# Performance work log

Measured on AMD Instinct MI355X. Metric: run time of the kernel, lower is better.

The kernel has to match this reference:

```python
import jax, jax.numpy as jnp
import numpy as np

BETA = 0.5

def gelu(x):
    return jax.nn.gelu(x, approximate=False)  # torch F.gelu default is exact erf

def setup_inputs() -> dict:
    key = jax.random.key(0)
    ks = jax.random.split(key, 10)
    N, F, PH, P, D, H, C, E = 50000, 128, 64, 8, 4, 128, 10, 1600000
    s = 0.05
    return {
        "x": jax.random.normal(ks[0], (N, F), jnp.float32),
        "W_proj": jax.random.normal(ks[1], (PH, F), jnp.float32) * s,
        "b_proj": jnp.zeros((PH,), jnp.float32),
        "W_x": jax.random.normal(ks[2], (H, F), jnp.float32) * s,
        "b_x": jnp.zeros((H,), jnp.float32),
        "W_path": jax.random.normal(ks[3], (H, D * PH), jnp.float32) * s,
        "b_path": jnp.zeros((H,), jnp.float32),
        "W_A": jax.random.normal(ks[4], (H, N), jnp.float32) * s,
        "b_A": jnp.zeros((H,), jnp.float32),
        "W_end": jax.random.normal(ks[5], (C, H), jnp.float32) * s,
        "b_end": jnp.zeros((C,), jnp.float32),
        "index": jax.random.randint(ks[6], (N, P, D), 0, N, jnp.int64)
                 if jax.config.jax_enable_x64 else jax.random.randint(ks[6], (N, P, D), 0, N, jnp.int32),
        "edge_index": jax.random.randint(ks[7], (2, E), 0, N, jnp.int32),
    }

def reference(x, W_proj, b_proj, W_x, b_x, W_path, b_path, W_A, b_A, W_end, b_end, index, edge_index):
    N = x.shape[0]
    # path projection then per-node path gather: [N, P, D, PH]
    pp = x @ W_proj.T + b_proj
    path = pp[index]
    Np, P, D, PH = path.shape
    # node MLP (dropout off in eval)
    h = gelu(x @ W_x.T + b_x)  # [N, H]
    # concat path encoder: [N, P, D*PH] -> [N, P, H]
    pi = gelu(path.reshape(Np, P, D * PH) @ W_path.T + b_path)
    # dot-product path attention with softmax over path dim
    att = jax.nn.softmax(jnp.einsum('nh,nph->np', h, pi), axis=-1)
    path_agg = jnp.einsum('np,nph->nh', att, pi)
    # sparse adjacency (COO, weights=1) times Linear weight: A @ W_A.T + b_A
    M = W_A.T  # [N, H]
    A_x = jax.ops.segment_sum(M[edge_index[1]], edge_index[0], num_segments=N) + b_A
    out = (1.0 - BETA) * (path_agg + h) + BETA * A_x
    out = gelu(out)
    return out @ W_end.T + b_end
```

## Files before the change

kernel.cpp:

```cpp
#include <hip/hip_runtime.h>
#include <hip/hip_bf16.h>
#include <math.h>

#define NF   128
#define NPH  64
#define NP   8
#define ND   4
#define NH   128
#define NC   10
#define BCAP 2560

typedef __bf16 bf16;
typedef __attribute__((ext_vector_type(4))) __bf16 bf16x4;
typedef __attribute__((ext_vector_type(8))) __bf16 bf16x8;
typedef __attribute__((ext_vector_type(4))) float f32x4;

template<int CTRL>
__device__ __forceinline__ float dpp_add(float x) {
    int t = __builtin_amdgcn_update_dpp(0, __float_as_int(x), CTRL, 0xf, 0xf, false);
    return x + __int_as_float(t);
}
__device__ __forceinline__ float row16_sum(float x) {
    x = dpp_add<0x121>(x);
    x = dpp_add<0x122>(x);
    x = dpp_add<0x124>(x);
    x = dpp_add<0x128>(x);
    return x;
}

__device__ __forceinline__ float gelu_fast(float x) {
    float z = fabsf(x) * 0.70710678118654752f;
    float t = __builtin_amdgcn_rcpf(1.0f + 0.47047f * z);
    float poly = t * (0.3480242f + t * (-0.0958798f + t * 0.7478556f));
    float erfv = 1.0f - poly * __expf(-z * z);
    float s = copysignf(erfv, x);
    return 0.5f * x * (1.0f + s);
}

#define GLOAD_LDS16(g, l)                                                     \
    __builtin_amdgcn_global_load_lds(                                         \
        (const __attribute__((address_space(1))) unsigned int*)(g),           \
        (__attribute__((address_space(3))) unsigned int*)(l), 16, 0, 0)

__device__ __forceinline__ bf16x8 cvt8(float4 a, float4 b) {
    bf16x8 r;
    r[0] = (bf16)a.x; r[1] = (bf16)a.y; r[2] = (bf16)a.z; r[3] = (bf16)a.w;
    r[4] = (bf16)b.x; r[5] = (bf16)b.y; r[6] = (bf16)b.z; r[7] = (bf16)b.w;
    return r;
}

__global__ __launch_bounds__(256) void k_front(
    const float* __restrict__ x,
    const float* __restrict__ Wproj, const float* __restrict__ bproj,
    const float* __restrict__ Wx,    const float* __restrict__ bx,
    bf16* __restrict__ pp, float* __restrict__ h,
    const float* __restrict__ WA, bf16* __restrict__ Mb,
    const int* __restrict__ esrc, const int* __restrict__ edst,
    int* __restrict__ gcur, unsigned* __restrict__ pairs,
    int N, int E, int nbuck, int nbP, int nbT)
{
    __shared__ alignas(16) char smem[33280];
    const int tid = threadIdx.x;

    const int bid = blockIdx.x;
    const int two = 2 * nbP;
    int cls, idx;
    if (bid < two) { cls = bid & 1; idx = bid >> 1; }
    else           { cls = 1; idx = nbP + (bid - two); }

    if (cls == 0) {
        bf16* x_s = (bf16*)smem;
        const int w = tid >> 6, l = tid & 63;
        const int c = l & 15, g = l >> 4;

        bf16x8 bfr[3][4];
        float bias[3];
        #pragma unroll
        for (int t = 0; t < 3; ++t) {
            int ch = (w * 3 + t) * 16 + c;
            const float* wr = (ch < NPH) ? &Wproj[(size_t)ch * NF]
                                         : &Wx[(size_t)(ch - NPH) * NF];
            bias[t] = (ch < NPH) ? bproj[ch] : bx[ch - NPH];
            #pragma unroll
            for (int ks = 0; ks < 4; ++ks) {
                const float* src = wr + ks * 32 + g * 8;
                bfr[t][ks] = cvt8(*(const float4*)src, *(const float4*)(src + 4));
            }
        }

        const int n0 = idx * 64;
        #pragma unroll
        for (int rr = 0; rr < 8; ++rr) {
            int id  = rr * 256 + tid;
            int row = id >> 5, c4 = id & 31;
            float4 v = make_float4(0.f, 0.f, 0.f, 0.f);
            if (n0 + row < N) v = *(const float4*)&x[(size_t)(n0 + row) * NF + c4 * 4];
            bf16x4 o;
            o[0] = (bf16)v.x; o[1] = (bf16)v.y; o[2] = (bf16)v.z; o[3] = (bf16)v.w;
            *(bf16x4*)&x_s[row * 136 + c4 * 4] = o;
        }
        __syncthreads();

        f32x4 acc[4][3] = {};
        #pragma unroll
        for (int rt = 0; rt < 4; ++rt)
            #pragma unroll
            for (int ks = 0; ks < 4; ++ks) {
                bf16x8 a = *(const bf16x8*)&x_s[(rt * 16 + c) * 136 + ks * 32 + g * 8];
                #pragma unroll
                for (int t = 0; t < 3; ++t)
                    acc[rt][t] = __builtin_amdgcn_mfma_f32_16x16x32_bf16(
                        a, bfr[t][ks], acc[rt][t], 0, 0, 0);
            }

        #pragma unroll
        for (int rt = 0; rt < 4; ++rt) {
            #pragma unroll
            for (int t = 0; t < 3; ++t) {
                int ch = (w * 3 + t) * 16 + c;
                #pragma unroll
                for (int i = 0; i < 4; ++i) {
                    int n = n0 + rt * 16 + g * 4 + i;
                    if (n >= N) continue;
                    float v = acc[rt][t][i] + bias[t];
                    if (ch < NPH) pp[(size_t)n * NPH + ch] = (bf16)v;
                    else          h[(size_t)n * NH + (ch - NPH)] = gelu_fast(v);
                }
            }
        }
    } else if (idx < nbT) {
        float* tt = (float*)smem;
        const int n0 = idx * 64;
        const int w = tid >> 6, l = tid & 63;
        #pragma unroll
        for (int rep = 0; rep < 32; ++rep) {
            int hh = rep * 4 + w;
            int n  = n0 + l;
            tt[hh * 65 + l] = (n < N) ? WA[(size_t)hh * N + n] : 0.f;
        }
        __syncthreads();
        #pragma unroll
        for (int rep = 0; rep < 32; ++rep) {
            int n_l = rep * 2 + (tid >> 7);
            int n   = n0 + n_l;
            if (n < N) Mb[(size_t)n * NH + (tid & 127)] = (bf16)tt[(tid & 127) * 65 + n_l];
        }
    } else {
        int* cnt  = (int*)smem;
        int* bofs = cnt + 800;
        const int tile = (idx - nbT) * 4096;
        for (int i = tid; i < nbuck; i += 256) cnt[i] = 0;
        __syncthreads();
        #pragma unroll
        for (int k = 0; k < 16; ++k) {
            int i = tile + k * 256 + tid;
            if (i < E) atomicAdd(&cnt[esrc[i] >> 6], 1);
        }
        __syncthreads();
        for (int i = tid; i < nbuck; i += 256) {
            int c = cnt[i];
            bofs[i] = c ? atomicAdd(&gcur[i], c) : 0;
            cnt[i] = 0;
        }
        __syncthreads();
        #pragma unroll
        for (int k = 0; k < 16; ++k) {
            int i = tile + k * 256 + tid;
            if (i < E) {
                int s = esrc[i], b = s >> 6;
                int r = atomicAdd(&cnt[b], 1);
                pairs[(size_t)b * BCAP + bofs[b] + r] =
                    ((unsigned)(s & 63) << 16) | (unsigned)edst[i];
            }
        }
    }
}

__global__ __launch_bounds__(256) void k_ax(
    const unsigned* __restrict__ pairs, const int* __restrict__ gcur,
    const bf16* __restrict__ Mb, const float* __restrict__ bA,
    float* __restrict__ axbuf2, int N)
{
    __shared__ int hist[64], sc[64], cur[64];
    __shared__ unsigned short dstl[BCAP];
    const int bid = blockIdx.x;
    const int ct  = bid & 3;
    const int b   = bid >> 2;
    const int t   = threadIdx.x;
    const int cnt = gcur[b];
    const unsigned* pb = pairs + (size_t)b * BCAP;

    if (t < 64) hist[t] = 0;
    __syncthreads();
    for (int j = t; j < cnt; j += 256)
        atomicAdd(&hist[pb[j] >> 16], 1);
    __syncthreads();
    if (t < 64) sc[t] = hist[t];
    __syncthreads();
    for (int off = 1; off < 64; off <<= 1) {
        int u = (t < 64 && t >= off) ? sc[t - off] : 0;
        __syncthreads();
        if (t < 64) sc[t] += u;
        __syncthreads();
    }
    if (t < 64) cur[t] = sc[t] - hist[t];
    __syncthreads();
    for (int j = t; j < cnt; j += 256) {
        unsigned p = pb[j];
        int pos = atomicAdd(&cur[p >> 16], 1);
        dstl[pos] = (unsigned short)(p & 0xffffu);
    }
    __syncthreads();

    const int w = t >> 6, l = t & 63;
    const int e = l >> 4, q = l & 15;
    const unsigned* Mu32 = (const unsigned*)Mb;
    const int dwbase = ct * 16;
    const int chb = ct * 32;
    const int nb0 = b * 64;
    const float bA0 = bA[chb + q * 2];
    const float bA1 = bA[chb + q * 2 + 1];

    #pragma unroll 1
    for (int it = 0; it < 16; ++it) {
        const int node = it * 4 + w;
        const int hi2 = sc[node];
        int j = hi2 - hist[node];
        float a0 = 0.f, a1 = 0.f;
        for (; j + 16 <= hi2; j += 16) {
            int d0 = dstl[j + e], d1 = dstl[j + 4 + e];
            int d2 = dstl[j + 8 + e], d3 = dstl[j + 12 + e];
            unsigned v0 = Mu32[(size_t)d0 * 64 + dwbase + q];
            unsigned v1 = Mu32[(size_t)d1 * 64 + dwbase + q];
            unsigned v2 = Mu32[(size_t)d2 * 64 + dwbase + q];
            unsigned v3 = Mu32[(size_t)d3 * 64 + dwbase + q];
            a0 += __uint_as_float(v0 << 16) + __uint_as_float(v1 << 16) +
                  __uint_as_float(v2 << 16) + __uint_as_float(v3 << 16);
            a1 += __uint_as_float(v0 & 0xffff0000u) + __uint_as_float(v1 & 0xffff0000u) +
                  __uint_as_float(v2 & 0xffff0000u) + __uint_as_float(v3 & 0xffff0000u);
        }
        for (; j + 4 <= hi2; j += 4) {
            int d0 = dstl[j + e];
            unsigned v0 = Mu32[(size_t)d0 * 64 + dwbase + q];
            a0 += __uint_as_float(v0 << 16);
            a1 += __uint_as_float(v0 & 0xffff0000u);
        }
        if (j + e < hi2) {
            int d0 = dstl[j + e];
            unsigned v0 = Mu32[(size_t)d0 * 64 + dwbase + q];
            a0 += __uint_as_float(v0 << 16);
            a1 += __uint_as_float(v0 & 0xffff0000u);
        }
        a0 += __shfl_xor(a0, 16, 64);  a0 += __shfl_xor(a0, 32, 64);
        a1 += __shfl_xor(a1, 16, 64);  a1 += __shfl_xor(a1, 32, 64);
        const int n = nb0 + node;
        if (l < 16 && n < N) {
            float2 o;
            o.x = 0.5f * (a0 + bA0);
            o.y = 0.5f * (a1 + bA1);
            *(float2*)&axbuf2[(size_t)n * NH + chb + q * 2] = o;
        }
    }
}

__global__ __launch_bounds__(256, 3) void k_path(
    const bf16* __restrict__ pp, const float* __restrict__ h,
    const float* __restrict__ Wpath, const float* __restrict__ bpath,
    const int* __restrict__ index, float* __restrict__ aggbuf,
    int N, int nrounds)
{
    __shared__ alignas(16) char smem[37376];
    bf16*  path_s = (bf16*)smem;
    float* h_sf   = (float*)(smem + 32768);
    float* s_red  = (float*)(smem + 36864);

    const int tid = threadIdx.x;
    const int w   = tid >> 6;
    const int l   = tid & 63;
    const int c   = l & 15;
    const int g   = l >> 4;
    const int nl  = g >> 1;

    bf16x8 bfrag[2][8];
    #pragma unroll
    for (int ht = 0; ht < 2; ++ht) {
        int hg = (w * 2 + ht) * 16 + c;
        #pragma unroll
        for (int ks = 0; ks < 8; ++ks) {
            const float* src = &Wpath[(size_t)hg * 256 + ks * 32 + g * 8];
            bfrag[ht][ks] = cvt8(*(const float4*)src, *(const float4*)(src + 4));
        }
    }
    const float bp0 = bpath[(w * 2 + 0) * 16 + c];
    const float bp1 = bpath[(w * 2 + 1) * 16 + c];

    auto stage = [&](int round, int b) {
        const int n0 = round * 4;
        #pragma unroll
        for (int rr = 0; rr < 4; ++rr) {
            int id  = rr * 256 + tid;
            int row = id >> 5;
            int cc  = id & 31;
            int ls  = cc ^ (row & 7);
            int d   = ls >> 3, q = ls & 7;
            int nn  = row >> 3, p = row & 7;
            int idx = index[(size_t)(n0 + nn) * (NP * ND) + p * ND + d];
            GLOAD_LDS16(pp + (size_t)idx * NPH + q * 8, &path_s[b * 8192 + id * 8]);
        }
        if (tid < 128) {
            int node = tid >> 5, q = tid & 31;
            GLOAD_LDS16(&h[(size_t)(n0 + node) * NH + q * 4],
                        &h_sf[(b * 4 + node) * 128 + q * 4]);
        }
    };

    int r = blockIdx.x;
    const int G = gridDim.x;
    if (r < nrounds) stage(r, 0);
    int buf = 0;

    for (; r < nrounds; r += G) {
        const int n0 = r * 4;
        __syncthreads();
        if (r + G < nrounds) stage(r + G, buf ^ 1);

        f32x4 acc[2][2] = {};
        #pragma unroll
        for (int rt = 0; rt < 2; ++rt) {
            const int rowbase = buf * 8192 + (rt * 16 + c) * 256;
            #pragma unroll
            for (int ks = 0; ks < 8; ++ks) {
                int chunk = (ks * 4 + g) ^ (c & 7);
                bf16x8 a = *(const bf16x8*)&path_s[rowbase + chunk * 8];
                acc[rt][0] = __builtin_amdgcn_mfma_f32_16x16x32_bf16(
                    a, bfrag[0][ks], acc[rt][0], 0, 0, 0);
                acc[rt][1] = __builtin_amdgcn_mfma_f32_16x16x32_bf16(
                    a, bfrag[1][ks], acc[rt][1], 0, 0, 0);
            }
        }

        float pi[2][2][4];
        #pragma unroll
        for (int rt = 0; rt < 2; ++rt) {
            const float hv0 = h_sf[(buf * 4 + rt * 2 + nl) * 128 + w * 32 + c];
            const float hv1 = h_sf[(buf * 4 + rt * 2 + nl) * 128 + w * 32 + 16 + c];
            float sp[4];
            #pragma unroll
            for (int i = 0; i < 4; ++i) {
                pi[rt][0][i] = gelu_fast(acc[rt][0][i] + bp0);
                pi[rt][1][i] = gelu_fast(acc[rt][1][i] + bp1);
                sp[i] = hv0 * pi[rt][0][i] + hv1 * pi[rt][1][i];
            }
            #pragma unroll
            for (int i = 0; i < 4; ++i) sp[i] = row16_sum(sp[i]);
            float v = (c == 0) ? sp[0] : (c == 1) ? sp[1] : (c == 2) ? sp[2] : sp[3];
            if (c < 4) s_red[w * 32 + rt * 16 + g * 4 + c] = v;
        }

        __builtin_amdgcn_sched_barrier(0);
        asm volatile("s_waitcnt lgkmcnt(0)" ::: "memory");
        __builtin_amdgcn_s_barrier();
        __builtin_amdgcn_sched_barrier(0);

        #pragma unroll
        for (int rt = 0; rt < 2; ++rt) {
            float4 r0 = *(const float4*)&s_red[0 * 32 + rt * 16 + g * 4];
            float4 r1 = *(const float4*)&s_red[1 * 32 + rt * 16 + g * 4];
            float4 r2 = *(const float4*)&s_red[2 * 32 + rt * 16 + g * 4];
            float4 r3 = *(const float4*)&s_red[3 * 32 + rt * 16 + g * 4];
            float st[4];
            st[0] = r0.x + r1.x + r2.x + r3.x;
            st[1] = r0.y + r1.y + r2.y + r3.y;
            st[2] = r0.z + r1.z + r2.z + r3.z;
            st[3] = r0.w + r1.w + r2.w + r3.w;
            float m4 = fmaxf(fmaxf(st[0], st[1]), fmaxf(st[2], st[3]));
            float m  = fmaxf(m4, __shfl_xor(m4, 16, 64));
            float e[4], s4 = 0.f;
            #pragma unroll
            for (int i = 0; i < 4; ++i) { e[i] = __expf(st[i] - m); s4 += e[i]; }
            float den = s4 + __shfl_xor(s4, 16, 64);
            const float inv = __builtin_amdgcn_rcpf(den);

            float pa0 = 0.f, pa1 = 0.f;
            #pragma unroll
            for (int i = 0; i < 4; ++i) {
                pa0 += e[i] * pi[rt][0][i];
                pa1 += e[i] * pi[rt][1][i];
            }
            pa0 = (pa0 + __shfl_xor(pa0, 16, 64)) * inv;
            pa1 = (pa1 + __shfl_xor(pa1, 16, 64)) * inv;

            if (!(g & 1)) {
                int n = n0 + rt * 2 + nl;
                const float hv0 = h_sf[(buf * 4 + rt * 2 + nl) * 128 + w * 32 + c];
                const float hv1 = h_sf[(buf * 4 + rt * 2 + nl) * 128 + w * 32 + 16 + c];
                aggbuf[(size_t)n * NH + w * 32 + c]      = 0.5f * (pa0 + hv0);
                aggbuf[(size_t)n * NH + w * 32 + 16 + c] = 0.5f * (pa1 + hv1);
            }
        }
        buf ^= 1;
    }
}

__global__ __launch_bounds__(256) void k_fin(
    const float* __restrict__ aggbuf, const float* __restrict__ axbuf2,
    const float* __restrict__ Wend, const float* __restrict__ bend,
    float* __restrict__ out, int N)
{
    __shared__ float wend_s[NC][128];
    __shared__ float bend_s[NC];
    const int tid = threadIdx.x;
    for (int id = tid; id < NC * 128; id += 256) wend_s[id >> 7][id & 127] = Wend[id];
    if (tid < NC) bend_s[tid] = bend[tid];
    __syncthreads();

    const int w = tid >> 6, l = tid & 63;
    const int n = blockIdx.x * 4 + w;
    if (n >= N) return;
    const int q = l & 15;

    float4 agA = *(const float4*)&aggbuf[(size_t)n * NH + q * 8];
    float4 agB = *(const float4*)&aggbuf[(size_t)n * NH + q * 8 + 4];
    float4 axA = *(const float4*)&axbuf2[(size_t)n * NH + q * 8];
    float4 axB = *(const float4*)&axbuf2[(size_t)n * NH + q * 8 + 4];
    float gg[8];
    gg[0] = gelu_fast(agA.x + axA.x);
    gg[1] = gelu_fast(agA.y + axA.y);
    gg[2] = gelu_fast(agA.z + axA.z);
    gg[3] = gelu_fast(agA.w + axA.w);
    gg[4] = gelu_fast(agB.x + axB.x);
    gg[5] = gelu_fast(agB.y + axB.y);
    gg[6] = gelu_fast(agB.z + axB.z);
    gg[7] = gelu_fast(agB.w + axB.w);

    float part[NC];
    #pragma unroll
    for (int cc = 0; cc < NC; ++cc) {
        float p = 0.f;
        #pragma unroll
        for (int k = 0; k < 8; ++k) p += gg[k] * wend_s[cc][q * 8 + k];
        part[cc] = row16_sum(p);
    }

    float r = part[0];
    #pragma unroll
    for (int cc = 1; cc < NC; ++cc) r = (l == cc) ? part[cc] : r;
    if (l < NC) out[(size_t)n * NC + l] = r + bend_s[l];
}

extern "C" void kernel_launch(void* const* d_in, const int* in_sizes, int n_in,
                              void* d_out, int out_size, void* d_ws, size_t ws_size,
                              hipStream_t stream)
{
    const float* x     = (const float*)d_in[0];
    const float* Wproj = (const float*)d_in[1];
    const float* bproj = (const float*)d_in[2];
    const float* Wx    = (const float*)d_in[3];
    const float* bx    = (const float*)d_in[4];
    const float* Wpath = (const float*)d_in[5];
    const float* bpath = (const float*)d_in[6];
    const float* WA    = (const float*)d_in[7];
    const float* bA    = (const float*)d_in[8];
    const float* Wend  = (const float*)d_in[9];
    const float* bend  = (const float*)d_in[10];
    const int*   index = (const int*)d_in[11];
    const int*   eidx  = (const int*)d_in[12];

    const int N = in_sizes[0] / NF;
    const int E = in_sizes[12] / 2;
    const int* esrc = eidx;
    const int* edst = eidx + E;
    const int nbuck = (N + 63) >> 6;

    char* p = (char*)d_ws;
    auto alloc = [&](size_t bytes) {
        char* r = p;
        p += (bytes + 255) & ~(size_t)255;
        return r;
    };
    bf16*     pp     = (bf16*)alloc((size_t)N * NPH * sizeof(bf16));
    float*    h      = (float*)alloc((size_t)N * NH * sizeof(float));
    float*    aggbuf = (float*)alloc((size_t)N * NH * sizeof(float));
    float*    axbuf2 = (float*)alloc((size_t)N * NH * sizeof(float));
    bf16*     Mb     = (bf16*)alloc((size_t)N * NH * sizeof(bf16));
    unsigned* pairs  = (unsigned*)alloc((size_t)nbuck * BCAP * sizeof(unsigned));
    int*      gcur   = (int*)alloc((size_t)nbuck * sizeof(int));

    const int nbP = (N + 63) / 64;
    const int nbT = (N + 63) / 64;
    const int nbB = (E + 4095) / 4096;
    const int NPATH = 1024;
    const int nrounds = N / 4;

    hipMemsetAsync(gcur, 0, (size_t)nbuck * sizeof(int), stream);
    k_front<<<nbP + nbT + nbB, 256, 0, stream>>>(
        x, Wproj, bproj, Wx, bx, pp, h, WA, Mb, esrc, edst, gcur, pairs,
        N, E, nbuck, nbP, nbT);
    k_ax<<<nbuck * 4, 256, 0, stream>>>(pairs, gcur, Mb, bA, axbuf2, N);
    k_path<<<NPATH, 256, 0, stream>>>(pp, h, Wpath, bpath, index, aggbuf, N, nrounds);
    k_fin<<<(N + 3) / 4, 256, 0, stream>>>(aggbuf, axbuf2, Wend, bend,
                                           (float*)d_out, N);
}
```

Baseline: 250.2 us.

## Fuse final GELU and output projection into path kernel; split front kernel

```diff
diff --git a/kernel.cpp b/kernel.cpp
--- a/kernel.cpp
+++ b/kernel.cpp
@@ -49,129 +49,132 @@
     return r;
 }
 
-__global__ __launch_bounds__(256) void k_front(
+__global__ __launch_bounds__(256) void k_proj(
     const float* __restrict__ x,
     const float* __restrict__ Wproj, const float* __restrict__ bproj,
     const float* __restrict__ Wx,    const float* __restrict__ bx,
-    bf16* __restrict__ pp, float* __restrict__ h,
-    const float* __restrict__ WA, bf16* __restrict__ Mb,
+    bf16* __restrict__ pp, float* __restrict__ h, int N)
+{
+    __shared__ alignas(16) bf16 x_s[64 * 136];
+    const int tid = threadIdx.x;
+    const int w = tid >> 6, l = tid & 63;
+    const int c = l & 15, g = l >> 4;
+
+    bf16x8 bfr[3][4];
+    float bias[3];
+    #pragma unroll
+    for (int t = 0; t < 3; ++t) {
+        int ch = (w * 3 + t) * 16 + c;
+        const float* wr = (ch < NPH) ? &Wproj[(size_t)ch * NF]
+                                     : &Wx[(size_t)(ch - NPH) * NF];
+        bias[t] = (ch < NPH) ? bproj[ch] : bx[ch - NPH];
+        #pragma unroll
+        for (int ks = 0; ks < 4; ++ks) {
+            const float* src = wr + ks * 32 + g * 8;
+            bfr[t][ks] = cvt8(*(const float4*)src, *(const float4*)(src + 4));
+        }
+    }
+
+    const int n0 = blockIdx.x * 64;
+    #pragma unroll
+    for (int rr = 0; rr < 8; ++rr) {
+        int id  = rr * 256 + tid;
+        int row = id >> 5, c4 = id & 31;
+        float4 v = make_float4(0.f, 0.f, 0.f, 0.f);
+        if (n0 + row < N) v = *(const float4*)&x[(size_t)(n0 + row) * NF + c4 * 4];
+        bf16x4 o;
+        o[0] = (bf16)v.x; o[1] = (bf16)v.y; o[2] = (bf16)v.z; o[3] = (bf16)v.w;
+        *(bf16x4*)&x_s[row * 136 + c4 * 4] = o;
+    }
+    __syncthreads();
+
+    f32x4 acc[4][3] = {};
+    #pragma unroll
+    for (int rt = 0; rt < 4; ++rt)
+        #pragma unroll
+        for (int ks = 0; ks < 4; ++ks) {
+            bf16x8 a = *(const bf16x8*)&x_s[(rt * 16 + c) * 136 + ks * 32 + g * 8];
+            #pragma unroll
+            for (int t = 0; t < 3; ++t)
+                acc[rt][t] = __builtin_amdgcn_mfma_f32_16x16x32_bf16(
+                    a, bfr[t][ks], acc[rt][t], 0, 0, 0);
+        }
+
+    #pragma unroll
+    for (int rt = 0; rt < 4; ++rt) {
+        #pragma unroll
+        for (int t = 0; t < 3; ++t) {
+            int ch = (w * 3 + t) * 16 + c;
+            #pragma unroll
+            for (int i = 0; i < 4; ++i) {
+                int n = n0 + rt * 16 + g * 4 + i;
+                if (n >= N) continue;
+                float v = acc[rt][t][i] + bias[t];
+                if (ch < NPH) pp[(size_t)n * NPH + ch] = (bf16)v;
+                else          h[(size_t)n * NH + (ch - NPH)] = gelu_fast(v);
+            }
+        }
+    }
+}
+
+__global__ __launch_bounds__(256) void k_transpose(
+    const float* __restrict__ WA, bf16* __restrict__ Mb, int N)
+{
+    __shared__ float tt[128][65];
+    const int n0  = blockIdx.x * 64;
+    const int tid = threadIdx.x;
+    const int w = tid >> 6, l = tid & 63;
+    #pragma unroll
+    for (int rep = 0; rep < 32; ++rep) {
+        int hh = rep * 4 + w;
+        int n  = n0 + l;
+        tt[hh][l] = (n < N) ? WA[(size_t)hh * N + n] : 0.f;
+    }
+    __syncthreads();
+    #pragma unroll
+    for (int rep = 0; rep < 32; ++rep) {
+        int n_l = rep * 2 + (tid >> 7);
+        int n   = n0 + n_l;
+        if (n < N) Mb[(size_t)n * NH + (tid & 127)] = (bf16)tt[tid & 127][n_l];
+    }
+}
+
+__global__ __launch_bounds__(256) void k_bucket(
     const int* __restrict__ esrc, const int* __restrict__ edst,
     int* __restrict__ gcur, unsigned* __restrict__ pairs,
-    int N, int E, int nbuck, int nbP, int nbT)
-{
-    __shared__ alignas(16) char smem[33280];
+    int E, int nbuck)
+{
+    __shared__ int cnt[1024];
+    __shared__ int bofs[1024];
     const int tid = threadIdx.x;
-
-    const int bid = blockIdx.x;
-    const int two = 2 * nbP;
-    int cls, idx;
-    if (bid < two) { cls = bid & 1; idx = bid >> 1; }
-    else           { cls = 1; idx = nbP + (bid - two); }
-
-    if (cls == 0) {
-        bf16* x_s = (bf16*)smem;
-        const int w = tid >> 6, l = tid & 63;
-        const int c = l & 15, g = l >> 4;
-
-        bf16x8 bfr[3][4];
-        float bias[3];
-        #pragma unroll
-        for (int t = 0; t < 3; ++t) {
-            int ch = (w * 3 + t) * 16 + c;
-            const float* wr = (ch < NPH) ? &Wproj[(size_t)ch * NF]
-                                         : &Wx[(size_t)(ch - NPH) * NF];
-            bias[t] = (ch < NPH) ? bproj[ch] : bx[ch - NPH];
-            #pragma unroll
-            for (int ks = 0; ks < 4; ++ks) {
-                const float* src = wr + ks * 32 + g * 8;
-                bfr[t][ks] = cvt8(*(const float4*)src, *(const float4*)(src + 4));
-            }
-        }
-
-        const int n0 = idx * 64;
-        #pragma unroll
-        for (int rr = 0; rr < 8; ++rr) {
-            int id  = rr * 256 + tid;
-            int row = id >> 5, c4 = id & 31;
-            float4 v = make_float4(0.f, 0.f, 0.f, 0.f);
-            if (n0 + row < N) v = *(const float4*)&x[(size_t)(n0 + row) * NF + c4 * 4];
-            bf16x4 o;
-            o[0] = (bf16)v.x; o[1] = (bf16)v.y; o[2] = (bf16)v.z; o[3] = (bf16)v.w;
-            *(bf16x4*)&x_s[row * 136 + c4 * 4] = o;
-        }
-        __syncthreads();
-
-        f32x4 acc[4][3] = {};
-        #pragma unroll
-        for (int rt = 0; rt < 4; ++rt)
-            #pragma unroll
-            for (int ks = 0; ks < 4; ++ks) {
-                bf16x8 a = *(const bf16x8*)&x_s[(rt * 16 + c) * 136 + ks * 32 + g * 8];
-                #pragma unroll
-                for (int t = 0; t < 3; ++t)
-                    acc[rt][t] = __builtin_amdgcn_mfma_f32_16x16x32_bf16(
-                        a, bfr[t][ks], acc[rt][t], 0, 0, 0);
-            }
-
-        #pragma unroll
-        for (int rt = 0; rt < 4; ++rt) {
-            #pragma unroll
-            for (int t = 0; t < 3; ++t) {
-                int ch = (w * 3 + t) * 16 + c;
-                #pragma unroll
-                for (int i = 0; i < 4; ++i) {
-                    int n = n0 + rt * 16 + g * 4 + i;
-                    if (n >= N) continue;
-                    float v = acc[rt][t][i] + bias[t];
-                    if (ch < NPH) pp[(size_t)n * NPH + ch] = (bf16)v;
-                    else          h[(size_t)n * NH + (ch - NPH)] = gelu_fast(v);
-                }
-            }
-        }
-    } else if (idx < nbT) {
-        float* tt = (float*)smem;
-        const int n0 = idx * 64;
-        const int w = tid >> 6, l = tid & 63;
-        #pragma unroll
-        for (int rep = 0; rep < 32; ++rep) {
-            int hh = rep * 4 + w;
-            int n  = n0 + l;
-            tt[hh * 65 + l] = (n < N) ? WA[(size_t)hh * N + n] : 0.f;
-        }
-        __syncthreads();
-        #pragma unroll
-        for (int rep = 0; rep < 32; ++rep) {
-            int n_l = rep * 2 + (tid >> 7);
-            int n   = n0 + n_l;
-            if (n < N) Mb[(size_t)n * NH + (tid & 127)] = (bf16)tt[(tid & 127) * 65 + n_l];
-        }
-    } else {
-        int* cnt  = (int*)smem;
-        int* bofs = cnt + 800;
-        const int tile = (idx - nbT) * 4096;
-        for (int i = tid; i < nbuck; i += 256) cnt[i] = 0;
-        __syncthreads();
-        #pragma unroll
-        for (int k = 0; k < 16; ++k) {
-            int i = tile + k * 256 + tid;
-            if (i < E) atomicAdd(&cnt[esrc[i] >> 6], 1);
-        }
-        __syncthreads();
-        for (int i = tid; i < nbuck; i += 256) {
+    const int tile = blockIdx.x * 4096;
+    for (int i = tid; i < nbuck; i += 256) cnt[i] = 0;
+    __syncthreads();
+    #pragma unroll
+    for (int k = 0; k < 16; ++k) {
+        int i = tile + k * 256 + tid;
+        if (i < E) atomicAdd(&cnt[esrc[i] >> 6], 1);
+    }
+    __syncthreads();
+    const unsigned off = ((unsigned)blockIdx.x * 197u) & 1023u;
+    #pragma unroll
+    for (int k = 0; k < 4; ++k) {
+        int i = (int)(((unsigned)tid + 256u * (unsigned)k + off) & 1023u);
+        if (i < nbuck) {
             int c = cnt[i];
             bofs[i] = c ? atomicAdd(&gcur[i], c) : 0;
             cnt[i] = 0;
         }
-        __syncthreads();
-        #pragma unroll
-        for (int k = 0; k < 16; ++k) {
-            int i = tile + k * 256 + tid;
-            if (i < E) {
-                int s = esrc[i], b = s >> 6;
-                int r = atomicAdd(&cnt[b], 1);
-                pairs[(size_t)b * BCAP + bofs[b] + r] =
-                    ((unsigned)(s & 63) << 16) | (unsigned)edst[i];
-            }
+    }
+    __syncthreads();
+    #pragma unroll
+    for (int k = 0; k < 16; ++k) {
+        int i = tile + k * 256 + tid;
+        if (i < E) {
+            int s = esrc[i], b = s >> 6;
+            int r = atomicAdd(&cnt[b], 1);
+            pairs[(size_t)b * BCAP + bofs[b] + r] =
+                ((unsigned)(s & 63) << 16) | (unsigned)edst[i];
         }
     }
 }
@@ -266,13 +269,15 @@
 __global__ __launch_bounds__(256, 3) void k_path(
     const bf16* __restrict__ pp, const float* __restrict__ h,
     const float* __restrict__ Wpath, const float* __restrict__ bpath,
-    const int* __restrict__ index, float* __restrict__ aggbuf,
-    int N, int nrounds)
-{
-    __shared__ alignas(16) char smem[37376];
+    const int* __restrict__ index, const float* __restrict__ axbuf2,
+    const float* __restrict__ Wend, const float* __restrict__ bend,
+    float* __restrict__ out, int N, int nrounds)
+{
+    __shared__ alignas(16) char smem[38144];
     bf16*  path_s = (bf16*)smem;
     float* h_sf   = (float*)(smem + 32768);
     float* s_red  = (float*)(smem + 36864);
+    float* s_fin  = (float*)(smem + 37376);
 
     const int tid = threadIdx.x;
     const int w   = tid >> 6;
@@ -293,6 +298,13 @@
     }
     const float bp0 = bpath[(w * 2 + 0) * 16 + c];
     const float bp1 = bpath[(w * 2 + 1) * 16 + c];
+
+    float wendr[NC][2];
+    #pragma unroll
+    for (int cc = 0; cc < NC; ++cc) {
+        wendr[cc][0] = Wend[cc * NH + w * 32 + c];
+        wendr[cc][1] = Wend[cc * NH + w * 32 + 16 + c];
+    }
 
     auto stage = [&](int round, int b) {
         const int n0 = round * 4;
@@ -324,6 +336,14 @@
         __syncthreads();
         if (r + G < nrounds) stage(r + G, buf ^ 1);
 
+        float axv[2][2];
+        #pragma unroll
+        for (int rt = 0; rt < 2; ++rt) {
+            int n = n0 + rt * 2 + nl;
+            axv[rt][0] = axbuf2[(size_t)n * NH + w * 32 + c];
+            axv[rt][1] = axbuf2[(size_t)n * NH + w * 32 + 16 + c];
+        }
+
         f32x4 acc[2][2] = {};
         #pragma unroll
         for (int rt = 0; rt < 2; ++rt) {
@@ -340,10 +360,12 @@
         }
 
         float pi[2][2][4];
+        float hvs[2][2];
         #pragma unroll
         for (int rt = 0; rt < 2; ++rt) {
             const float hv0 = h_sf[(buf * 4 + rt * 2 + nl) * 128 + w * 32 + c];
             const float hv1 = h_sf[(buf * 4 + rt * 2 + nl) * 128 + w * 32 + 16 + c];
+            hvs[rt][0] = hv0; hvs[rt][1] = hv1;
             float sp[4];
             #pragma unroll
             for (int i = 0; i < 4; ++i) {
@@ -390,62 +412,38 @@
             pa0 = (pa0 + __shfl_xor(pa0, 16, 64)) * inv;
             pa1 = (pa1 + __shfl_xor(pa1, 16, 64)) * inv;
 
-            if (!(g & 1)) {
-                int n = n0 + rt * 2 + nl;
-                const float hv0 = h_sf[(buf * 4 + rt * 2 + nl) * 128 + w * 32 + c];
-                const float hv1 = h_sf[(buf * 4 + rt * 2 + nl) * 128 + w * 32 + 16 + c];
-                aggbuf[(size_t)n * NH + w * 32 + c]      = 0.5f * (pa0 + hv0);
-                aggbuf[(size_t)n * NH + w * 32 + 16 + c] = 0.5f * (pa1 + hv1);
+            float g0 = gelu_fast(0.5f * (pa0 + hvs[rt][0]) + axv[rt][0]);
+            float g1 = gelu_fast(0.5f * (pa1 + hvs[rt][1]) + axv[rt][1]);
+            float part[NC];
+            #pragma unroll
+            for (int cc = 0; cc < NC; ++cc)
+                part[cc] = g0 * wendr[cc][0] + g1 * wendr[cc][1];
+            #pragma unroll
+            for (int cc = 0; cc < NC; ++cc) part[cc] = row16_sum(part[cc]);
+            if (((g & 1) == 0) && c == 0) {
+                float* dst = &s_fin[((rt * 2 + nl) * 4 + w) * 12];
+                #pragma unroll
+                for (int cc = 0; cc < NC; ++cc) dst[cc] = part[cc];
+            }
+        }
+
+        __builtin_amdgcn_sched_barrier(0);
+        asm volatile("s_waitcnt lgkmcnt(0)" ::: "memory");
+        __builtin_amdgcn_s_barrier();
+        __builtin_amdgcn_sched_barrier(0);
+
+        if (tid < 64) {
+            int node = tid >> 4, idx = tid & 15;
+            if (idx < NC) {
+                float rs = s_fin[(node * 4 + 0) * 12 + idx]
+                         + s_fin[(node * 4 + 1) * 12 + idx]
+                         + s_fin[(node * 4 + 2) * 12 + idx]
+                         + s_fin[(node * 4 + 3) * 12 + idx];
+                out[(size_t)(n0 + node) * NC + idx] = rs + bend[idx];
             }
         }
         buf ^= 1;
     }
-}
-
-__global__ __launch_bounds__(256) void k_fin(
-    const float* __restrict__ aggbuf, const float* __restrict__ axbuf2,
-    const float* __restrict__ Wend, const float* __restrict__ bend,
-    float* __restrict__ out, int N)
-{
-    __shared__ float wend_s[NC][128];
-    __shared__ float bend_s[NC];
-    const int tid = threadIdx.x;
-    for (int id = tid; id < NC * 128; id += 256) wend_s[id >> 7][id & 127] = Wend[id];
-    if (tid < NC) bend_s[tid] = bend[tid];
-    __syncthreads();
-
-    const int w = tid >> 6, l = tid & 63;
-    const int n = blockIdx.x * 4 + w;
-    if (n >= N) return;
-    const int q = l & 15;
-
-    float4 agA = *(const float4*)&aggbuf[(size_t)n * NH + q * 8];
-    float4 agB = *(const float4*)&aggbuf[(size_t)n * NH + q * 8 + 4];
-    float4 axA = *(const float4*)&axbuf2[(size_t)n * NH + q * 8];
-    float4 axB = *(const float4*)&axbuf2[(size_t)n * NH + q * 8 + 4];
-    float gg[8];
-    gg[0] = gelu_fast(agA.x + axA.x);
-    gg[1] = gelu_fast(agA.y + axA.y);
-    gg[2] = gelu_fast(agA.z + axA.z);
-    gg[3] = gelu_fast(agA.w + axA.w);
-    gg[4] = gelu_fast(agB.x + axB.x);
-    gg[5] = gelu_fast(agB.y + axB.y);
-    gg[6] = gelu_fast(agB.z + axB.z);
-    gg[7] = gelu_fast(agB.w + axB.w);
-
-    float part[NC];
-    #pragma unroll
-    for (int cc = 0; cc < NC; ++cc) {
-        float p = 0.f;
-        #pragma unroll
-        for (int k = 0; k < 8; ++k) p += gg[k] * wend_s[cc][q * 8 + k];
-        part[cc] = row16_sum(p);
-    }
-
-    float r = part[0];
-    #pragma unroll
-    for (int cc = 1; cc < NC; ++cc) r = (l == cc) ? part[cc] : r;
-    if (l < NC) out[(size_t)n * NC + l] = r + bend_s[l];
 }
 
 extern "C" void kernel_launch(void* const* d_in, const int* in_sizes, int n_in,
@@ -480,7 +478,6 @@
     };
     bf16*     pp     = (bf16*)alloc((size_t)N * NPH * sizeof(bf16));
     float*    h      = (float*)alloc((size_t)N * NH * sizeof(float));
-    float*    aggbuf = (float*)alloc((size_t)N * NH * sizeof(float));
     float*    axbuf2 = (float*)alloc((size_t)N * NH * sizeof(float));
     bf16*     Mb     = (bf16*)alloc((size_t)N * NH * sizeof(bf16));
     unsigned* pairs  = (unsigned*)alloc((size_t)nbuck * BCAP * sizeof(unsigned));
@@ -493,11 +490,10 @@
     const int nrounds = N / 4;
 
     hipMemsetAsync(gcur, 0, (size_t)nbuck * sizeof(int), stream);
-    k_front<<<nbP + nbT + nbB, 256, 0, stream>>>(
-        x, Wproj, bproj, Wx, bx, pp, h, WA, Mb, esrc, edst, gcur, pairs,
-        N, E, nbuck, nbP, nbT);
+    k_proj<<<nbP, 256, 0, stream>>>(x, Wproj, bproj, Wx, bx, pp, h, N);
+    k_transpose<<<nbT, 256, 0, stream>>>(WA, Mb, N);
+    k_bucket<<<nbB, 256, 0, stream>>>(esrc, edst, gcur, pairs, E, nbuck);
     k_ax<<<nbuck * 4, 256, 0, stream>>>(pairs, gcur, Mb, bA, axbuf2, N);
-    k_path<<<NPATH, 256, 0, stream>>>(pp, h, Wpath, bpath, index, aggbuf, N, nrounds);
-    k_fin<<<(N + 3) / 4, 256, 0, stream>>>(aggbuf, axbuf2, Wend, bend,
-                                           (float*)d_out, N);
-}
+    k_path<<<NPATH, 256, 0, stream>>>(pp, h, Wpath, bpath, index, axbuf2,
+                                      Wend, bend, (float*)d_out, N, nrounds);
+}
```

New measurement: 273.4 us. 9.3% more time.
